# Optimization experiments

Hardware: AMD Instinct MI355X
Metric: run time of the kernel (lower is better)

Reference implementation:

```python
import jax, jax.numpy as jnp
import numpy as np

BETA = 0.25


def setup_inputs() -> dict:
    key = jax.random.key(0)
    k1, k2 = jax.random.split(key)
    inputs = jax.random.normal(k1, (16, 64, 64, 256), dtype=jnp.float32)
    # codebook, shape (embedding_dim=256, num_embeddings=1024), uniform init like tf
    embeddings = jax.random.uniform(k2, (256, 1024), dtype=jnp.float32)
    return {"inputs": inputs, "embeddings": embeddings}


def reference(inputs, embeddings):
    D = embeddings.shape[0]
    flat = inputs.reshape(-1, D)  # [N, D]
    distances = (
        jnp.sum(flat * flat, axis=1, keepdims=True)
        - 2.0 * (flat @ embeddings)
        + jnp.sum(embeddings * embeddings, axis=0, keepdims=True)
    )
    encoding_indices = jnp.argmin(distances, axis=1)  # == argmax(-d)
    # one_hot @ embeddings.T is just a row gather from the codebook
    quantized = jnp.take(embeddings.T, encoding_indices, axis=0).reshape(inputs.shape)
    commitment_loss = BETA * jnp.mean(
        (jax.lax.stop_gradient(quantized) - inputs) ** 2
    )
    # straight-through estimator
    quantized = inputs + jax.lax.stop_gradient(quantized - inputs)
    return quantized, commitment_loss, encoding_indices
```

## Files before the change

kernel.cpp:

```cpp
#include <hip/hip_runtime.h>
#include <float.h>

typedef _Float16 half8 __attribute__((ext_vector_type(8)));
typedef float    f32x4 __attribute__((ext_vector_type(4)));

#define N_ROWS   65536
#define DIM      256
#define KCODES   1024
#define VQ_BETA  0.25
#define MARGIN   1.5f
#define HCAP     640

__global__ void transpose_e(const float* __restrict__ E, float* __restrict__ Et) {
    __shared__ float t[32][33];
    const int kt = blockIdx.x * 32;
    const int dt = blockIdx.y * 32;
    const int lx = threadIdx.x & 31;
    const int ly = threadIdx.x >> 5;
#pragma unroll
    for (int i = 0; i < 4; ++i) {
        int d = dt + ly + i * 8;
        t[ly + i * 8][lx] = E[(size_t)d * KCODES + kt + lx];
    }
    __syncthreads();
#pragma unroll
    for (int i = 0; i < 4; ++i) {
        int k = kt + ly + i * 8;
        Et[(size_t)k * DIM + dt + lx] = t[lx][ly + i * 8];
    }
}

__global__ void enorm_kernel(const float* __restrict__ E, float* __restrict__ enorm) {
    const int k = blockIdx.x * 256 + threadIdx.x;
    float s = 0.f;
#pragma unroll 4
    for (int d = 0; d < DIM; ++d) {
        float v = E[(size_t)d * KCODES + k];
        s = fmaf(v, v, s);
    }
    enorm[k] = s;
}

__global__ void efrag_kernel(const float* __restrict__ Et, _Float16* __restrict__ Efb) {
    const int fid = blockIdx.x * 256 + threadIdx.x;
    const int lhi   = fid & 3;
    const int llo   = (fid >> 2) & 15;
    const int nt    = (fid >> 6) & 3;
    const int w     = (fid >> 8) & 3;
    const int slice = fid >> 10;
    const int chunk = slice >> 3, ks = slice & 7;
    const int code  = chunk * 256 + w * 64 + nt * 16 + llo;
    const float* src = Et + (size_t)code * DIM + ks * 32 + lhi * 8;
    half8 h;
#pragma unroll
    for (int j = 0; j < 8; ++j) h[j] = (_Float16)src[j];
    *reinterpret_cast<half8*>(Efb + (size_t)fid * 8) = h;
}

__device__ __forceinline__ void load_bf2(const _Float16* __restrict__ eb,
                                         half8 (&bf)[2]) {
    bf[0] = *reinterpret_cast<const half8*>(eb);
    bf[1] = *reinterpret_cast<const half8*>(eb + 512);
}
__device__ __forceinline__ void load_af(const char* AhB, int ks, int llo, int lhi,
                                        int aswz, half8 (&af)[4]) {
#pragma unroll
    for (int mt = 0; mt < 4; ++mt) {
        const int addr = ((mt * 16 + llo) * 512 + (ks * 4 + lhi) * 16) ^ aswz;
        af[mt] = *reinterpret_cast<const half8*>(AhB + addr);
    }
}
__device__ __forceinline__ void mfma8(const half8 (&af)[4], const half8 (&bf)[2],
                                      f32x4 (&acc)[4][2]) {
#pragma unroll
    for (int mt = 0; mt < 4; ++mt)
#pragma unroll
        for (int nt = 0; nt < 2; ++nt)
            acc[mt][nt] = __builtin_amdgcn_mfma_f32_16x16x32_f16(
                af[mt], bf[nt], acc[mt][nt], 0, 0, 0);
}
__device__ __forceinline__ void mfma_chunk(
        const _Float16* __restrict__ ebase, const char* AhB,
        int llo, int lhi, int aswz, f32x4 (&acc)[4][2]) {
    half8 bfa[2], bfb[2], af[4];
    load_bf2(ebase, bfa);
#pragma unroll
    for (int ks2 = 0; ks2 < 4; ++ks2) {
        const int ksA = ks2 * 2, ksB = ks2 * 2 + 1;
        load_bf2(ebase + (size_t)ksB * 8192, bfb);
        load_af(AhB, ksA, llo, lhi, aswz, af);
        mfma8(af, bfa, acc);
        if (ksB < 7) load_bf2(ebase + (size_t)(ksB + 1) * 8192, bfa);
        load_af(AhB, ksB, llo, lhi, aswz, af);
        mfma8(af, bfb, acc);
    }
}

__global__ __launch_bounds__(512, 4) void vq_mfma(
        const float* __restrict__ X, const _Float16* __restrict__ Efb,
        const float* __restrict__ enorm, const float* __restrict__ Et,
        float* __restrict__ outidx, float* __restrict__ outq,
        float* __restrict__ partials)
{
    __shared__ _Float16 Ah[64 * 256];
    __shared__ float    bminw[8][64];
    __shared__ float    cutoff_s[64];
    __shared__ float    rmin_s[64];
    __shared__ unsigned minb[64], mini[64];
    __shared__ int      rowbad[64];
    __shared__ int      hits[HCAP];
    __shared__ float    dstore[HCAP];
    __shared__ unsigned hitcnt;

    const int tid = threadIdx.x;
    const int rowbase = blockIdx.x * 64;

    if (tid == 0) hitcnt = 0;
    if (tid < 64) {
        minb[tid] = 0xFFFFFFFFu; mini[tid] = 0xFFFFFFFFu;
        rmin_s[tid] = FLT_MAX;   rowbad[tid] = 0;
    }

    {
        const int row = tid >> 3;
#pragma unroll
        for (int i = 0; i < 4; ++i) {
            const int g = (tid & 7) + 8 * i;
            const float* src = X + (size_t)(rowbase + row) * DIM + g * 8;
            float4 a = *reinterpret_cast<const float4*>(src);
            float4 b = *reinterpret_cast<const float4*>(src + 4);
            half8 h;
            h[0] = (_Float16)a.x; h[1] = (_Float16)a.y;
            h[2] = (_Float16)a.z; h[3] = (_Float16)a.w;
            h[4] = (_Float16)b.x; h[5] = (_Float16)b.y;
            h[6] = (_Float16)b.z; h[7] = (_Float16)b.w;
            const int addr = (row * 512 + g * 16) ^ ((row & 7) << 4);
            *reinterpret_cast<half8*>(reinterpret_cast<char*>(Ah) + addr) = h;
        }
    }
    __syncthreads();

    const int w    = tid >> 6;
    const int lane = tid & 63;
    const int lhi  = lane >> 4, llo = lane & 15;
    const int aswz = (llo & 7) << 4;
    const int lane_off8 = (llo * 4 + lhi) * 8;
    const char* AhB = reinterpret_cast<const char*>(Ah);

    for (int chunk = 0; chunk < 4; ++chunk) {
        f32x4 acc[4][2];
#pragma unroll
        for (int mt = 0; mt < 4; ++mt)
#pragma unroll
            for (int nt = 0; nt < 2; ++nt) acc[mt][nt] = (f32x4){0.f, 0.f, 0.f, 0.f};

        const _Float16* ebase = Efb + (size_t)chunk * 65536 + w * 1024 + lane_off8;
        mfma_chunk(ebase, AhB, llo, lhi, aswz, acc);

        float e2v[2];
#pragma unroll
        for (int nt = 0; nt < 2; ++nt)
            e2v[nt] = enorm[chunk * 256 + w * 32 + nt * 16 + llo];

        float mloc[16];
#pragma unroll
        for (int mt = 0; mt < 4; ++mt)
#pragma unroll
            for (int q = 0; q < 4; ++q) {
                float m = FLT_MAX;
#pragma unroll
                for (int nt = 0; nt < 2; ++nt) {
                    const float ds = fmaf(-2.0f, acc[mt][nt][q], e2v[nt]);
                    acc[mt][nt][q] = ds;
                    m = fminf(m, ds);
                }
                mloc[mt * 4 + q] = m;
            }
#pragma unroll
        for (int m = 1; m < 16; m <<= 1)
#pragma unroll
            for (int sl = 0; sl < 16; ++sl)
                mloc[sl] = fminf(mloc[sl], __shfl_xor(mloc[sl], m, 64));
        if (llo == 0) {
#pragma unroll
            for (int mt = 0; mt < 4; ++mt)
#pragma unroll
                for (int q = 0; q < 4; ++q)
                    bminw[w][mt * 16 + lhi * 4 + q] = mloc[mt * 4 + q];
        }
        __syncthreads();
        if (tid < 64) {
            float r = bminw[0][tid];
#pragma unroll
            for (int ww = 1; ww < 8; ++ww) r = fminf(r, bminw[ww][tid]);
            r = fminf(rmin_s[tid], r);
            rmin_s[tid]   = r;
            cutoff_s[tid] = r + MARGIN;
        }
        __syncthreads();

#pragma unroll
        for (int mt = 0; mt < 4; ++mt)
#pragma unroll
            for (int q = 0; q < 4; ++q) {
                const int row = mt * 16 + lhi * 4 + q;
                const float cut = cutoff_s[row];
#pragma unroll
                for (int nt = 0; nt < 2; ++nt) {
                    if (acc[mt][nt][q] < cut) {
                        const unsigned p = atomicAdd(&hitcnt, 1u);
                        if (p < HCAP)
                            hits[p] = (row << 10) |
                                      (chunk * 256 + w * 32 + nt * 16 + llo);
                        else
                            rowbad[row] = 1;
                    }
                }
            }
    }
    __syncthreads();

    const int nh = (int)(hitcnt < HCAP ? hitcnt : (unsigned)HCAP);

    for (int hi = tid; hi < nh; hi += 512) {
        const int pk = hits[hi];
        const int rl = pk >> 10, code = pk & 1023;
        const float* xr = X  + (size_t)(rowbase + rl) * DIM;
        const float* er = Et + (size_t)code * DIM;
        float p = 0.f, x2 = 0.f;
#pragma unroll
        for (int j = 0; j < 64; ++j) {
            float4 xv = *reinterpret_cast<const float4*>(xr + j * 4);
            float4 ev = *reinterpret_cast<const float4*>(er + j * 4);
            x2 = fmaf(xv.x, xv.x, x2); x2 = fmaf(xv.y, xv.y, x2);
            x2 = fmaf(xv.z, xv.z, x2); x2 = fmaf(xv.w, xv.w, x2);
            p  = fmaf(xv.x, ev.x, p);  p  = fmaf(xv.y, ev.y, p);
            p  = fmaf(xv.z, ev.z, p);  p  = fmaf(xv.w, ev.w, p);
        }
        const float dd = (x2 - 2.0f * p) + enorm[code];
        dstore[hi] = dd;
        atomicMin(&minb[rl], __float_as_uint(dd));
    }
    __syncthreads();
    for (int hi = tid; hi < nh; hi += 512) {
        const int pk = hits[hi];
        const int rl = pk >> 10;
        if (__float_as_uint(dstore[hi]) == minb[rl])
            atomicMin(&mini[rl], (unsigned)(pk & 1023));
    }
    __syncthreads();

    float* xs = dstore;
    for (int r = 0; r < 64; ++r) {
        if (!rowbad[r]) continue;
        if (tid < 256) xs[tid] = X[(size_t)(rowbase + r) * DIM + tid];
        __syncthreads();
        if (tid < 256) {
            float x2 = 0.f;
            for (int d = 0; d < DIM; ++d) x2 = fmaf(xs[d], xs[d], x2);
            float a0 = 0.f, a1 = 0.f, a2 = 0.f, a3 = 0.f;
            const float* e0 = Et + (size_t)(tid      ) * DIM;
            const float* e1 = Et + (size_t)(tid + 256) * DIM;
            const float* e2p = Et + (size_t)(tid + 512) * DIM;
            const float* e3 = Et + (size_t)(tid + 768) * DIM;
            for (int d = 0; d < DIM; ++d) {
                const float xv = xs[d];
                a0 = fmaf(xv, e0[d], a0);
                a1 = fmaf(xv, e1[d], a1);
                a2 = fmaf(xv, e2p[d], a2);
                a3 = fmaf(xv, e3[d], a3);
            }
            const float d0 = (x2 - 2.0f * a0) + enorm[tid];
            const float d1 = (x2 - 2.0f * a1) + enorm[tid + 256];
            const float d2 = (x2 - 2.0f * a2) + enorm[tid + 512];
            const float d3 = (x2 - 2.0f * a3) + enorm[tid + 768];
            atomicMin(&minb[r], __float_as_uint(d0));
            atomicMin(&minb[r], __float_as_uint(d1));
            atomicMin(&minb[r], __float_as_uint(d2));
            atomicMin(&minb[r], __float_as_uint(d3));
            __syncthreads();
            const unsigned mb = minb[r];
            if (__float_as_uint(d0) == mb) atomicMin(&mini[r], (unsigned)tid);
            if (__float_as_uint(d1) == mb) atomicMin(&mini[r], (unsigned)(tid + 256));
            if (__float_as_uint(d2) == mb) atomicMin(&mini[r], (unsigned)(tid + 512));
            if (__float_as_uint(d3) == mb) atomicMin(&mini[r], (unsigned)(tid + 768));
        } else {
            __syncthreads();
        }
        __syncthreads();
    }

    float* red = dstore;
    {
        const int row  = tid >> 3;
        const int part = tid & 7;
        const int cw   = (int)mini[row];
        const float* xrow = X  + (size_t)(rowbase + row) * DIM;
        const float* ew   = Et + (size_t)cw * DIM;
        float* oq = outq + (size_t)(rowbase + row) * DIM;
        if (part == 0) outidx[rowbase + row] = (float)cw;

        float lsum = 0.f;
#pragma unroll
        for (int j = 0; j < 8; ++j) {
            const int d0 = j * 32 + part * 4;
            float4 q = *reinterpret_cast<const float4*>(ew + d0);
            float4 x = *reinterpret_cast<const float4*>(xrow + d0);
            float4 o;
            o.x = x.x + (q.x - x.x);
            o.y = x.y + (q.y - x.y);
            o.z = x.z + (q.z - x.z);
            o.w = x.w + (q.w - x.w);
            *reinterpret_cast<float4*>(oq + d0) = o;
            float dx;
            dx = q.x - x.x; lsum = fmaf(dx, dx, lsum);
            dx = q.y - x.y; lsum = fmaf(dx, dx, lsum);
            dx = q.z - x.z; lsum = fmaf(dx, dx, lsum);
            dx = q.w - x.w; lsum = fmaf(dx, dx, lsum);
        }
        __syncthreads();
        red[tid] = lsum;
    }
    __syncthreads();
    for (int s = 256; s > 0; s >>= 1) {
        if (tid < s) red[tid] += red[tid + s];
        __syncthreads();
    }
    if (tid == 0) partials[blockIdx.x] = red[0];
}

__global__ void loss_final(const float* __restrict__ partials, float* __restrict__ out) {
    __shared__ double sd[256];
    const int tid = threadIdx.x;
    double s = 0.0;
    for (int i = tid; i < 1024; i += 256) s += (double)partials[i];
    sd[tid] = s;
    __syncthreads();
    for (int k = 128; k > 0; k >>= 1) {
        if (tid < k) sd[tid] += sd[tid + k];
        __syncthreads();
    }
    if (tid == 0) out[0] = (float)(VQ_BETA * sd[0] / (double)((size_t)N_ROWS * DIM));
}

extern "C" void kernel_launch(void* const* d_in, const int* in_sizes, int n_in,
                              void* d_out, int out_size, void* d_ws, size_t ws_size,
                              hipStream_t stream) {
    const float* X = (const float*)d_in[0];
    const float* E = (const float*)d_in[1];

    float* outq    = (float*)d_out;
    float* outloss = outq + (size_t)N_ROWS * DIM;
    float* outidx  = outloss + 1;

    float*    Et       = (float*)d_ws;
    _Float16* Efb      = (_Float16*)(Et + 262144);
    float*    enormw   = (float*)(Efb + 262144);
    float*    partials = enormw + KCODES;

    transpose_e <<<dim3(32, 8), 256, 0, stream>>>(E, Et);
    enorm_kernel<<<4,           256, 0, stream>>>(E, enormw);
    efrag_kernel<<<128,         256, 0, stream>>>(Et, Efb);
    vq_mfma     <<<N_ROWS / 64, 512, 0, stream>>>(X, Efb, enormw, Et,
                                                  outidx, outq, partials);
    loss_final  <<<1,           256, 0, stream>>>(partials, outloss);
}
```

Before: 166.1 us.

## Replace per-chunk shuffle reduction and barriers with LDS atomicMin running row minima

The per-chunk row-minimum reduction (16-step xor shuffles, a shared staging array and two __syncthreads) is replaced by direct LDS atomicMin on order-preserving unsigned keys of the per-lane minimum. Each wave then reads whatever running minimum is available to form its cutoff, with no block barrier, so cutoffs can be looser and more candidates pass the filter. To absorb the extra hits, the hit buffer capacity is raised from 640 to 1536, which increases LDS use and may lower occupancy. The intent is to remove the shuffle work and the barrier stalls inside the chunk loop.

```diff
diff --git a/kernel.cpp b/kernel.cpp
--- a/kernel.cpp
+++ b/kernel.cpp
@@ -9,7 +9,17 @@
 #define KCODES   1024
 #define VQ_BETA  0.25
 #define MARGIN   1.5f
-#define HCAP     640
+#define HCAP     1536
+
+__device__ __forceinline__ unsigned fkey(float f) {
+    const unsigned u = __float_as_uint(f);
+    return u ^ (0x80000000u | (unsigned)((int)u >> 31));
+}
+__device__ __forceinline__ float funkey(unsigned k) {
+    const unsigned u = (k & 0x80000000u) ? (k ^ 0x80000000u) : ~k;
+    return __uint_as_float(u);
+}
+#define RMIN_INIT 0xFF7FFFFFu
 
 __global__ void transpose_e(const float* __restrict__ E, float* __restrict__ Et) {
     __shared__ float t[32][33];
@@ -103,9 +113,7 @@
         float* __restrict__ partials)
 {
     __shared__ _Float16 Ah[64 * 256];
-    __shared__ float    bminw[8][64];
-    __shared__ float    cutoff_s[64];
-    __shared__ float    rmin_s[64];
+    __shared__ unsigned rmink[64];
     __shared__ unsigned minb[64], mini[64];
     __shared__ int      rowbad[64];
     __shared__ int      hits[HCAP];
@@ -117,8 +125,9 @@
 
     if (tid == 0) hitcnt = 0;
     if (tid < 64) {
+        rmink[tid] = RMIN_INIT;
         minb[tid] = 0xFFFFFFFFu; mini[tid] = 0xFFFFFFFFu;
-        rmin_s[tid] = FLT_MAX;   rowbad[tid] = 0;
+        rowbad[tid] = 0;
     }
 
     {
@@ -162,7 +171,6 @@
         for (int nt = 0; nt < 2; ++nt)
             e2v[nt] = enorm[chunk * 256 + w * 32 + nt * 16 + llo];
 
-        float mloc[16];
 #pragma unroll
         for (int mt = 0; mt < 4; ++mt)
 #pragma unroll
@@ -174,37 +182,15 @@
                     acc[mt][nt][q] = ds;
                     m = fminf(m, ds);
                 }
-                mloc[mt * 4 + q] = m;
+                atomicMin(&rmink[mt * 16 + lhi * 4 + q], fkey(m));
             }
-#pragma unroll
-        for (int m = 1; m < 16; m <<= 1)
-#pragma unroll
-            for (int sl = 0; sl < 16; ++sl)
-                mloc[sl] = fminf(mloc[sl], __shfl_xor(mloc[sl], m, 64));
-        if (llo == 0) {
-#pragma unroll
-            for (int mt = 0; mt < 4; ++mt)
-#pragma unroll
-                for (int q = 0; q < 4; ++q)
-                    bminw[w][mt * 16 + lhi * 4 + q] = mloc[mt * 4 + q];
-        }
-        __syncthreads();
-        if (tid < 64) {
-            float r = bminw[0][tid];
-#pragma unroll
-            for (int ww = 1; ww < 8; ++ww) r = fminf(r, bminw[ww][tid]);
-            r = fminf(rmin_s[tid], r);
-            rmin_s[tid]   = r;
-            cutoff_s[tid] = r + MARGIN;
-        }
-        __syncthreads();
 
 #pragma unroll
         for (int mt = 0; mt < 4; ++mt)
 #pragma unroll
             for (int q = 0; q < 4; ++q) {
                 const int row = mt * 16 + lhi * 4 + q;
-                const float cut = cutoff_s[row];
+                const float cut = funkey(rmink[row]) + MARGIN;
 #pragma unroll
                 for (int nt = 0; nt < 2; ++nt) {
                     if (acc[mt][nt][q] < cut) {
```

After: 274.2 us. +65.1%, slower.
